# Kernel optimization log

Hardware: AMD Instinct MI355X
Metric: run time of the kernel (lower is better)

Reference implementation:

```python
import jax, jax.numpy as jnp
import numpy as np

N = 100000      # nodes
E = 1600000     # edges (avg degree 16)
IN, HID, OUT = 128, 128, 64


def setup_inputs() -> dict:
    key = jax.random.key(0)
    k1, k2, k3, k4 = jax.random.split(key, 4)
    x = jax.random.normal(k1, (N, IN), dtype=jnp.float32)
    edge_index = jax.random.randint(k2, (2, E), 0, N, dtype=jnp.int64)
    # GCNConv linear weights (glorot-ish scale) and zero biases
    W1 = jax.random.normal(k3, (IN, HID), dtype=jnp.float32) * (1.0 / np.sqrt(IN))
    b1 = jnp.zeros((HID,), jnp.float32)
    W2 = jax.random.normal(k4, (HID, OUT), dtype=jnp.float32) * (1.0 / np.sqrt(HID))
    b2 = jnp.zeros((OUT,), jnp.float32)
    return {"x": x, "edge_index": edge_index, "W1": W1, "b1": b1, "W2": W2, "b2": b2}


def reference(x, edge_index, W1, b1, W2, b2):
    n = x.shape[0]
    loops = jnp.arange(n, dtype=edge_index.dtype)
    self_e = jnp.stack([loops, loops])  # [2, N]
    # forward() explicitly adds self-loops, then PyG GCNConv's gcn_norm
    # (add_self_loops=True by default) adds a second set -> duplicate (i,i) edges.
    ei = jnp.concatenate([edge_index, self_e, self_e], axis=1)
    row, col = ei[0], ei[1]  # source, target

    # symmetric normalization: deg over target index, norm_e = d^-1/2[row]*d^-1/2[col]
    deg = jax.ops.segment_sum(jnp.ones(row.shape, x.dtype), col, num_segments=n)
    dis = jax.lax.rsqrt(deg)  # deg >= 2 thanks to self-loops
    norm = dis[row] * dis[col]  # [E']

    def gcn_conv(h, W, b):
        h = h @ W                               # transform first (PyG order)
        msg = h[row] * norm[:, None]            # gather + per-edge scale
        agg = jax.ops.segment_sum(msg, col, num_segments=n)  # scatter-add
        return agg + b

    h = jax.nn.relu(gcn_conv(x, W1, b1))
    return gcn_conv(h, W2, b2)
```

## Files before the change

### kernel.cpp

```cpp
#include <hip/hip_runtime.h>
#include <hip/hip_fp16.h>

#define NPB   512
#define NBMAX 256
#define CHUNK 2048

using f16x4 = __attribute__((ext_vector_type(4))) _Float16;
using f32x4 = __attribute__((ext_vector_type(4))) float;

__global__ void k_detect(const int* __restrict__ ei32, int* __restrict__ flag,
                         int* __restrict__ bcur, int nb, int cap) {
  int t = threadIdx.x;
  if (t < nb) bcur[t] = t * cap;
  if (t == 0) {
    int z = 1;
    for (int k = 0; k < 64; ++k)
      if (ei32[2 * k + 1] != 0) { z = 0; break; }
    flag[0] = z;
  }
}

__device__ __forceinline__ int edge_at(const void* ei, int is64, long long pos) {
  return is64 ? (int)((const long long*)ei)[pos] : ((const int*)ei)[pos];
}

__global__ __launch_bounds__(256) void k_fillB(const void* __restrict__ ei,
                                               const int* __restrict__ flag, int E,
                                               int* __restrict__ bcur,
                                               int* __restrict__ tmp, int nb) {
  __shared__ int cntL[NBMAX], startL[NBMAX], curL[NBMAX], gofs[NBMAX];
  __shared__ int sh[NBMAX];
  __shared__ int stage[CHUNK];
  __shared__ unsigned char sbkt[CHUNK];
  int t = threadIdx.x;
  int is64 = flag[0];
  long long base = (long long)blockIdx.x * CHUNK;
  if (base >= E) return;
  int m = (int)min((long long)CHUNK, (long long)E - base);
  cntL[t] = 0;
  __syncthreads();
  for (int i = t; i < m; i += 256) {
    int c = edge_at(ei, is64, (long long)E + base + i);
    atomicAdd(&cntL[c >> 9], 1);
  }
  __syncthreads();
  sh[t] = cntL[t];
  __syncthreads();
  for (int off = 1; off < NBMAX; off <<= 1) {
    int x = 0;
    if (t >= off) x = sh[t - off];
    __syncthreads();
    if (t >= off) sh[t] += x;
    __syncthreads();
  }
  int excl = t ? sh[t - 1] : 0;
  startL[t] = excl;
  curL[t] = excl;
  if (t < nb && cntL[t] > 0) gofs[t] = atomicAdd(&bcur[t], cntL[t]);
  __syncthreads();
  for (int i = t; i < m; i += 256) {
    int r = edge_at(ei, is64, base + i);
    int c = edge_at(ei, is64, (long long)E + base + i);
    int b = c >> 9;
    int p = atomicAdd(&curL[b], 1);
    stage[p] = ((c & 511) << 17) | r;
    sbkt[p] = (unsigned char)b;
  }
  __syncthreads();
  for (int i = t; i < m; i += 256) {
    int b = sbkt[i];
    tmp[gofs[b] + (i - startL[b])] = stage[i];
  }
}

template <int BN, bool AHALF, bool PRESCALE>
__device__ void gemm_body(char* smem, const void* __restrict__ Av,
                          const float* __restrict__ W,
                          const float* __restrict__ dis,
                          __half* __restrict__ C, int M, int tiles,
                          int bid, int nblk) {
  _Float16 (*Wt)[136] = (_Float16(*)[136])smem;
  _Float16 (*At)[136] = (_Float16(*)[136])(smem + sizeof(_Float16) * BN * 136);
  float* disL = (float*)(smem + sizeof(_Float16) * (BN + 64) * 136);
  constexpr int NT = BN / 64;
  constexpr int CH = BN / 4;
  int t = threadIdx.x;
  int lane = t & 63, w = t >> 6;
  int lrow = lane & 15;
  int kq = (lane >> 4) * 4;
  int wcol0 = w * (BN / 4);

  for (int idx = t; idx < 128 * BN / 4; idx += 256) {
    int k = idx / CH, c4 = (idx % CH) * 4;
    float4 v = *(const float4*)&W[(size_t)k * BN + c4];
    Wt[c4 + 0][k] = (_Float16)v.x;
    Wt[c4 + 1][k] = (_Float16)v.y;
    Wt[c4 + 2][k] = (_Float16)v.z;
    Wt[c4 + 3][k] = (_Float16)v.w;
  }

  for (int tile = bid; tile < tiles; tile += nblk) {
    int row0 = tile * 64;
    __syncthreads();
#pragma unroll
    for (int i = 0; i < 8; ++i) {
      int idx = t + i * 256;
      int r = idx >> 5, c = (idx & 31) * 4;
      int gr = row0 + r;
      f16x4 hv = {0, 0, 0, 0};
      if (gr < M) {
        if constexpr (AHALF) {
          hv = *(const f16x4*)&((const _Float16*)Av)[(size_t)gr * 128 + c];
        } else {
          float4 v = *(const float4*)&((const float*)Av)[(size_t)gr * 128 + c];
          hv = f16x4{(_Float16)v.x, (_Float16)v.y, (_Float16)v.z, (_Float16)v.w};
        }
      }
      *(f16x4*)&At[r][c] = hv;
    }
    if constexpr (PRESCALE) {
      if (t < 64) {
        int gr = row0 + t;
        disL[t] = (gr < M) ? dis[gr] : 0.f;
      }
    }
    __syncthreads();
    f32x4 acc[4][NT];
#pragma unroll
    for (int mt = 0; mt < 4; ++mt)
#pragma unroll
      for (int nt = 0; nt < NT; ++nt) acc[mt][nt] = f32x4{0.f, 0.f, 0.f, 0.f};
#pragma unroll
    for (int k0 = 0; k0 < 128; k0 += 16) {
      int kk = k0 + kq;
      f16x4 a[4], b[NT];
#pragma unroll
      for (int mt = 0; mt < 4; ++mt)
        a[mt] = *(const f16x4*)&At[mt * 16 + lrow][kk];
#pragma unroll
      for (int nt = 0; nt < NT; ++nt)
        b[nt] = *(const f16x4*)&Wt[wcol0 + nt * 16 + lrow][kk];
#pragma unroll
      for (int mt = 0; mt < 4; ++mt)
#pragma unroll
        for (int nt = 0; nt < NT; ++nt)
          acc[mt][nt] = __builtin_amdgcn_mfma_f32_16x16x16f16(a[mt], b[nt],
                                                              acc[mt][nt], 0, 0, 0);
    }
    __syncthreads();
#pragma unroll
    for (int mt = 0; mt < 4; ++mt)
#pragma unroll
      for (int nt = 0; nt < NT; ++nt) {
        int cc = wcol0 + nt * 16 + lrow;
        int rr = mt * 16 + kq;
#pragma unroll
        for (int reg = 0; reg < 4; ++reg) {
          float val = acc[mt][nt][reg];
          if constexpr (PRESCALE) val *= disL[rr + reg];
          At[rr + reg][cc] = (_Float16)val;
        }
      }
    __syncthreads();
#pragma unroll
    for (int i = 0; i < BN / 16; ++i) {
      int idx = t + i * 256;
      int r = idx / CH, c = (idx % CH) * 4;
      int gr = row0 + r;
      if (gr < M)
        *(f16x4*)&C[(size_t)gr * BN + c] = *(const f16x4*)&At[r][c];
    }
  }
}

__global__ __launch_bounds__(256) void k_gemm1(
    const void* __restrict__ x, const float* __restrict__ W1,
    __half* __restrict__ t1, int M, int tiles) {
  extern __shared__ char smem[];
  gemm_body<128, false, false>(smem, x, W1, nullptr, t1, M, tiles,
                               blockIdx.x, gridDim.x);
}

__global__ __launch_bounds__(256) void k_gemm2(
    const void* __restrict__ Av, const float* __restrict__ W,
    const float* __restrict__ dis, __half* __restrict__ C, int M, int tiles) {
  extern __shared__ char smem[];
  gemm_body<64, true, true>(smem, Av, W, dis, C, M, tiles, blockIdx.x, gridDim.x);
}

__global__ void k_bscan(const int* __restrict__ bcur, int cap,
                        int* __restrict__ bbase, int* __restrict__ rowptr,
                        int nb, int N, int E) {
  __shared__ int sh[NBMAX];
  int t = threadIdx.x;
  sh[t] = (t < nb) ? (bcur[t] - t * cap) : 0;
  __syncthreads();
  for (int off = 1; off < NBMAX; off <<= 1) {
    int x = 0;
    if (t >= off) x = sh[t - off];
    __syncthreads();
    if (t >= off) sh[t] += x;
    __syncthreads();
  }
  int excl = t ? sh[t - 1] : 0;
  if (t < nb) bbase[t] = excl;
  if (t == 0) { bbase[nb] = E; rowptr[N] = E; }
}

__global__ __launch_bounds__(256) void k_fillC(const int* __restrict__ tmp,
                                               const int* __restrict__ bcur,
                                               const int* __restrict__ bbase,
                                               int cap, int* __restrict__ rowptr,
                                               float* __restrict__ dis,
                                               int* __restrict__ esrc,
                                               __half* __restrict__ t1, int N) {
  __shared__ int cnt[NPB];
  __shared__ int loc[NPB];
  __shared__ float disS[NPB];
  __shared__ int sh[256];
  int b = blockIdx.x, t = threadIdx.x;
  int beg = b * cap;
  int end = bcur[b];
  int outb = bbase[b];
  int base_node = b << 9;
  cnt[t] = 0; cnt[t + 256] = 0;
  __syncthreads();
  for (int e = beg + t; e < end; e += 256)
    atomicAdd(&cnt[tmp[e] >> 17], 1);
  __syncthreads();
  int c0 = cnt[2 * t], c1 = cnt[2 * t + 1];
  sh[t] = c0 + c1;
  __syncthreads();
  for (int off = 1; off < 256; off <<= 1) {
    int x = 0;
    if (t >= off) x = sh[t - off];
    __syncthreads();
    if (t >= off) sh[t] += x;
    __syncthreads();
  }
  int pre = t ? sh[t - 1] : 0;
  loc[2 * t] = outb + pre;
  loc[2 * t + 1] = outb + pre + c0;
  float d0 = rsqrtf((float)(c0 + 2)), d1 = rsqrtf((float)(c1 + 2));
  disS[2 * t] = d0; disS[2 * t + 1] = d1;
  int v0 = base_node + 2 * t, v1 = v0 + 1;
  if (v0 < N) { rowptr[v0] = outb + pre;      dis[v0] = d0; }
  if (v1 < N) { rowptr[v1] = outb + pre + c0; dis[v1] = d1; }
  __syncthreads();
  for (int e = beg + t; e < end; e += 256) {
    int u = tmp[e];
    int pos = atomicAdd(&loc[u >> 17], 1);
    esrc[pos] = u & 0x1FFFF;
  }
  for (int idx = t; idx < NPB * 16; idx += 256) {
    int row = idx >> 4, ch = (idx & 15) * 8;
    int v = base_node + row;
    if (v < N) {
      size_t ofs = (size_t)v * 128 + ch;
      uint4 u = *(const uint4*)&t1[ofs];
      float dsc = disS[row];
      __half2* hp = (__half2*)&u;
#pragma unroll
      for (int j = 0; j < 4; ++j) {
        float lo = __low2float(hp[j]) * dsc, hi = __high2float(hp[j]) * dsc;
        hp[j] = __floats2half2_rn(lo, hi);
      }
      *(uint4*)&t1[ofs] = u;
    }
  }
}

#define ACC4(u)                                                         \
  { __half2 p;                                                          \
    p = *(__half2*)&(u).x; a0 += __low2float(p); a1 += __high2float(p); \
    p = *(__half2*)&(u).y; a2 += __low2float(p); a3 += __high2float(p); }

__global__ __launch_bounds__(256) void k_gather128(const __half* __restrict__ t,
    const float* __restrict__ bias, const int* __restrict__ rowptr,
    const int* __restrict__ esrc, const float* __restrict__ dis,
    __half* __restrict__ o, int n) {
  int gw = (int)((blockIdx.x * blockDim.x + threadIdx.x) >> 6);
  int lane = threadIdx.x & 63;
  int nw = (int)((gridDim.x * blockDim.x) >> 6);
  int half = lane >> 5;
  int f = (lane & 31) * 4;
  for (int v = gw; v < n; v += nw) {
    float a0 = 0.f, a1 = 0.f, a2 = 0.f, a3 = 0.f;
    int beg = rowptr[v], end = rowptr[v + 1];
    int e = beg + half;
    for (; e + 14 < end; e += 16) {
      int s0 = esrc[e],      s1 = esrc[e + 2],  s2 = esrc[e + 4],  s3 = esrc[e + 6];
      int s4 = esrc[e + 8],  s5 = esrc[e + 10], s6 = esrc[e + 12], s7 = esrc[e + 14];
      uint2 u0 = *(const uint2*)&t[(size_t)s0 * 128 + f];
      uint2 u1 = *(const uint2*)&t[(size_t)s1 * 128 + f];
      uint2 u2 = *(const uint2*)&t[(size_t)s2 * 128 + f];
      uint2 u3 = *(const uint2*)&t[(size_t)s3 * 128 + f];
      uint2 u4 = *(const uint2*)&t[(size_t)s4 * 128 + f];
      uint2 u5 = *(const uint2*)&t[(size_t)s5 * 128 + f];
      uint2 u6 = *(const uint2*)&t[(size_t)s6 * 128 + f];
      uint2 u7 = *(const uint2*)&t[(size_t)s7 * 128 + f];
      ACC4(u0) ACC4(u1) ACC4(u2) ACC4(u3)
      ACC4(u4) ACC4(u5) ACC4(u6) ACC4(u7)
    }
    for (; e + 6 < end; e += 8) {
      int s0 = esrc[e], s1 = esrc[e + 2], s2 = esrc[e + 4], s3 = esrc[e + 6];
      uint2 u0 = *(const uint2*)&t[(size_t)s0 * 128 + f];
      uint2 u1 = *(const uint2*)&t[(size_t)s1 * 128 + f];
      uint2 u2 = *(const uint2*)&t[(size_t)s2 * 128 + f];
      uint2 u3 = *(const uint2*)&t[(size_t)s3 * 128 + f];
      ACC4(u0) ACC4(u1) ACC4(u2) ACC4(u3)
    }
    for (; e < end; e += 2) {
      int s0 = esrc[e];
      uint2 u0 = *(const uint2*)&t[(size_t)s0 * 128 + f];
      ACC4(u0)
    }
    if (half == 0) {
      uint2 uv = *(const uint2*)&t[(size_t)v * 128 + f];
      __half2 p;
      p = *(__half2*)&uv.x; a0 = fmaf(2.f, __low2float(p), a0); a1 = fmaf(2.f, __high2float(p), a1);
      p = *(__half2*)&uv.y; a2 = fmaf(2.f, __low2float(p), a2); a3 = fmaf(2.f, __high2float(p), a3);
    }
    a0 += __shfl_xor(a0, 32); a1 += __shfl_xor(a1, 32);
    a2 += __shfl_xor(a2, 32); a3 += __shfl_xor(a3, 32);
    if (half == 0) {
      float dv = dis[v];
      a0 = fmaxf(fmaf(dv, a0, bias[f]),     0.f);
      a1 = fmaxf(fmaf(dv, a1, bias[f + 1]), 0.f);
      a2 = fmaxf(fmaf(dv, a2, bias[f + 2]), 0.f);
      a3 = fmaxf(fmaf(dv, a3, bias[f + 3]), 0.f);
      __half2 h0 = __floats2half2_rn(a0, a1), h1 = __floats2half2_rn(a2, a3);
      uint2 uu;
      uu.x = *(unsigned int*)&h0; uu.y = *(unsigned int*)&h1;
      *(uint2*)&o[(size_t)v * 128 + f] = uu;
    }
  }
}

__global__ __launch_bounds__(256) void k_gather64(const __half* __restrict__ t,
    const float* __restrict__ bias, const int* __restrict__ rowptr,
    const int* __restrict__ esrc, const float* __restrict__ dis,
    float* __restrict__ o, int n) {
  int gw = (int)((blockIdx.x * blockDim.x + threadIdx.x) >> 6);
  int lane = threadIdx.x & 63;
  int nw = (int)((gridDim.x * blockDim.x) >> 6);
  int sub = lane >> 4;
  int f = (lane & 15) * 4;
  for (int v = gw; v < n; v += nw) {
    float a0 = 0.f, a1 = 0.f, a2 = 0.f, a3 = 0.f;
    int beg = rowptr[v], end = rowptr[v + 1];
    int e = beg + sub;
    for (; e + 12 < end; e += 16) {
      int s0 = esrc[e], s1 = esrc[e + 4], s2 = esrc[e + 8], s3 = esrc[e + 12];
      uint2 u0 = *(const uint2*)&t[(size_t)s0 * 64 + f];
      uint2 u1 = *(const uint2*)&t[(size_t)s1 * 64 + f];
      uint2 u2 = *(const uint2*)&t[(size_t)s2 * 64 + f];
      uint2 u3 = *(const uint2*)&t[(size_t)s3 * 64 + f];
      ACC4(u0) ACC4(u1) ACC4(u2) ACC4(u3)
    }
    for (; e < end; e += 4) {
      int s0 = esrc[e];
      uint2 u0 = *(const uint2*)&t[(size_t)s0 * 64 + f];
      ACC4(u0)
    }
    if (sub == 0) {
      uint2 uv = *(const uint2*)&t[(size_t)v * 64 + f];
      __half2 p;
      p = *(__half2*)&uv.x; a0 = fmaf(2.f, __low2float(p), a0); a1 = fmaf(2.f, __high2float(p), a1);
      p = *(__half2*)&uv.y; a2 = fmaf(2.f, __low2float(p), a2); a3 = fmaf(2.f, __high2float(p), a3);
    }
    a0 += __shfl_xor(a0, 16); a0 += __shfl_xor(a0, 32);
    a1 += __shfl_xor(a1, 16); a1 += __shfl_xor(a1, 32);
    a2 += __shfl_xor(a2, 16); a2 += __shfl_xor(a2, 32);
    a3 += __shfl_xor(a3, 16); a3 += __shfl_xor(a3, 32);
    if (sub == 0) {
      float dv = dis[v];
      float4 r;
      r.x = fmaf(dv, a0, bias[f]);     r.y = fmaf(dv, a1, bias[f + 1]);
      r.z = fmaf(dv, a2, bias[f + 2]); r.w = fmaf(dv, a3, bias[f + 3]);
      *(float4*)&o[(size_t)v * 64 + f] = r;
    }
  }
}

extern "C" void kernel_launch(void* const* d_in, const int* in_sizes, int n_in,
                              void* d_out, int out_size, void* d_ws, size_t ws_size,
                              hipStream_t stream) {
  const float* x  = (const float*)d_in[0];
  const void*  ei = d_in[1];
  const float* W1 = (const float*)d_in[2];
  const float* b1 = (const float*)d_in[3];
  const float* W2 = (const float*)d_in[4];
  const float* b2 = (const float*)d_in[5];
  const int N = in_sizes[0] / 128;
  const int E = in_sizes[1] / 2;
  float* out = (float*)d_out;
  const int nb  = (N + NPB - 1) / NPB;
  const int cap = E / nb + 4096;

  size_t off = 0;
  auto alloc = [&](size_t bytes) -> void* {
    void* p = (char*)d_ws + off;
    off += (bytes + 255) & ~(size_t)255;
    return p;
  };
  int*    flag   = (int*)alloc(4);
  int*    bcur   = (int*)alloc(NBMAX * 4);
  int*    bbase  = (int*)alloc((NBMAX + 1) * 4);
  int*    rowptr = (int*)alloc(((size_t)N + 1) * 4);
  float*  dis    = (float*)alloc((size_t)N * 4);
  int*    tmp    = (int*)alloc(((size_t)nb * cap + 16384) * 4);
  int*    esrc   = (int*)alloc((size_t)E * 4);
  __half* t1     = (__half*)alloc((size_t)N * 128 * 2);
  __half* z1     = (__half*)alloc((size_t)N * 128 * 2);
  __half* t2     = t1;

  int tiles = (N + 63) / 64;
  int nchunks = (E + CHUNK - 1) / CHUNK;
  const int smem_gemm1 = (128 + 64) * 136 * 2 + 256;
  const int smem_gemm2 = (64 + 64) * 136 * 2 + 256;

  k_detect<<<1, 256, 0, stream>>>((const int*)ei, flag, bcur, nb, cap);
  k_gemm1<<<768, 256, smem_gemm1, stream>>>(x, W1, t1, N, tiles);
  k_fillB<<<nchunks, 256, 0, stream>>>(ei, flag, E, bcur, tmp, nb);
  k_bscan<<<1, 256, 0, stream>>>(bcur, cap, bbase, rowptr, nb, N, E);
  k_fillC<<<nb, 256, 0, stream>>>(tmp, bcur, bbase, cap, rowptr, dis, esrc, t1, N);

  k_gather128<<<2048, 256, 0, stream>>>(t1, b1, rowptr, esrc, dis, z1, N);
  k_gemm2<<<min(tiles, 768), 256, smem_gemm2, stream>>>(z1, W2, dis, t2, N, tiles);
  k_gather64<<<2048, 256, 0, stream>>>(t2, b2, rowptr, esrc, dis, out, N);
}
```

Baseline: 230.7 us.

## Move GEMM1 after CSR build with fused dis prescale and register-resident W

GEMM1 now runs after the CSR/degree build, so it can apply the dis[row] prescale in its epilogue. This removes the separate read-modify-write pass over t1 that k_fillC used to do. The GEMM kernel is rewritten so each wave holds its W fragments in registers rather than in a shared-memory transposed tile, uses BN*4 threads, and launches one block per tile. The trade-off is that GEMM1 can no longer overlap with the CSR build and must wait for dis, and W is loaded with strided scalar global reads.

```diff
diff --git a/kernel.cpp b/kernel.cpp
--- a/kernel.cpp
+++ b/kernel.cpp
@@ -73,38 +73,100 @@
   }
 }
 
+__global__ void k_bscan(const int* __restrict__ bcur, int cap,
+                        int* __restrict__ bbase, int* __restrict__ rowptr,
+                        int nb, int N, int E) {
+  __shared__ int sh[NBMAX];
+  int t = threadIdx.x;
+  sh[t] = (t < nb) ? (bcur[t] - t * cap) : 0;
+  __syncthreads();
+  for (int off = 1; off < NBMAX; off <<= 1) {
+    int x = 0;
+    if (t >= off) x = sh[t - off];
+    __syncthreads();
+    if (t >= off) sh[t] += x;
+    __syncthreads();
+  }
+  int excl = t ? sh[t - 1] : 0;
+  if (t < nb) bbase[t] = excl;
+  if (t == 0) { bbase[nb] = E; rowptr[N] = E; }
+}
+
+__global__ __launch_bounds__(256) void k_fillC(const int* __restrict__ tmp,
+                                               const int* __restrict__ bcur,
+                                               const int* __restrict__ bbase,
+                                               int cap, int* __restrict__ rowptr,
+                                               float* __restrict__ dis,
+                                               int* __restrict__ esrc, int N) {
+  __shared__ int cnt[NPB];
+  __shared__ int loc[NPB];
+  __shared__ int sh[256];
+  int b = blockIdx.x, t = threadIdx.x;
+  int beg = b * cap;
+  int end = bcur[b];
+  int outb = bbase[b];
+  int base_node = b << 9;
+  cnt[t] = 0; cnt[t + 256] = 0;
+  __syncthreads();
+  for (int e = beg + t; e < end; e += 256)
+    atomicAdd(&cnt[tmp[e] >> 17], 1);
+  __syncthreads();
+  int c0 = cnt[2 * t], c1 = cnt[2 * t + 1];
+  sh[t] = c0 + c1;
+  __syncthreads();
+  for (int off = 1; off < 256; off <<= 1) {
+    int x = 0;
+    if (t >= off) x = sh[t - off];
+    __syncthreads();
+    if (t >= off) sh[t] += x;
+    __syncthreads();
+  }
+  int pre = t ? sh[t - 1] : 0;
+  loc[2 * t] = outb + pre;
+  loc[2 * t + 1] = outb + pre + c0;
+  int v0 = base_node + 2 * t, v1 = v0 + 1;
+  if (v0 < N) { rowptr[v0] = outb + pre;      dis[v0] = rsqrtf((float)(c0 + 2)); }
+  if (v1 < N) { rowptr[v1] = outb + pre + c0; dis[v1] = rsqrtf((float)(c1 + 2)); }
+  __syncthreads();
+  for (int e = beg + t; e < end; e += 256) {
+    int u = tmp[e];
+    int pos = atomicAdd(&loc[u >> 17], 1);
+    esrc[pos] = u & 0x1FFFF;
+  }
+}
+
 template <int BN, bool AHALF, bool PRESCALE>
-__device__ void gemm_body(char* smem, const void* __restrict__ Av,
-                          const float* __restrict__ W,
-                          const float* __restrict__ dis,
-                          __half* __restrict__ C, int M, int tiles,
-                          int bid, int nblk) {
-  _Float16 (*Wt)[136] = (_Float16(*)[136])smem;
-  _Float16 (*At)[136] = (_Float16(*)[136])(smem + sizeof(_Float16) * BN * 136);
-  float* disL = (float*)(smem + sizeof(_Float16) * (BN + 64) * 136);
-  constexpr int NT = BN / 64;
+__global__ __launch_bounds__(BN * 4) void k_gemm(const void* __restrict__ Av,
+                                                 const float* __restrict__ W,
+                                                 const float* __restrict__ dis,
+                                                 __half* __restrict__ C,
+                                                 int M, int tiles) {
+  constexpr int THREADS = BN * 4;
   constexpr int CH = BN / 4;
+  __shared__ _Float16 At[64][136];
+  __shared__ float disL[64];
   int t = threadIdx.x;
   int lane = t & 63, w = t >> 6;
   int lrow = lane & 15;
   int kq = (lane >> 4) * 4;
-  int wcol0 = w * (BN / 4);
-
-  for (int idx = t; idx < 128 * BN / 4; idx += 256) {
-    int k = idx / CH, c4 = (idx % CH) * 4;
-    float4 v = *(const float4*)&W[(size_t)k * BN + c4];
-    Wt[c4 + 0][k] = (_Float16)v.x;
-    Wt[c4 + 1][k] = (_Float16)v.y;
-    Wt[c4 + 2][k] = (_Float16)v.z;
-    Wt[c4 + 3][k] = (_Float16)v.w;
-  }
-
-  for (int tile = bid; tile < tiles; tile += nblk) {
+  int col = w * 16 + lrow;
+
+  f16x4 bfrag[8];
+#pragma unroll
+  for (int k8 = 0; k8 < 8; ++k8) {
+    int kb = k8 * 16 + kq;
+    bfrag[k8] = f16x4{(_Float16)W[(size_t)(kb + 0) * BN + col],
+                      (_Float16)W[(size_t)(kb + 1) * BN + col],
+                      (_Float16)W[(size_t)(kb + 2) * BN + col],
+                      (_Float16)W[(size_t)(kb + 3) * BN + col]};
+  }
+
+  for (int tile = blockIdx.x; tile < tiles; tile += gridDim.x) {
     int row0 = tile * 64;
     __syncthreads();
 #pragma unroll
-    for (int i = 0; i < 8; ++i) {
-      int idx = t + i * 256;
+    for (int i = 0; i < (64 * 32) / THREADS; ++i) {
+      int idx = t + i * THREADS;
       int r = idx >> 5, c = (idx & 31) * 4;
       int gr = row0 + r;
       f16x4 hv = {0, 0, 0, 0};
@@ -125,147 +187,40 @@
       }
     }
     __syncthreads();
-    f32x4 acc[4][NT];
-#pragma unroll
-    for (int mt = 0; mt < 4; ++mt)
-#pragma unroll
-      for (int nt = 0; nt < NT; ++nt) acc[mt][nt] = f32x4{0.f, 0.f, 0.f, 0.f};
-#pragma unroll
-    for (int k0 = 0; k0 < 128; k0 += 16) {
-      int kk = k0 + kq;
-      f16x4 a[4], b[NT];
+    f32x4 acc[4];
+#pragma unroll
+    for (int mt = 0; mt < 4; ++mt) acc[mt] = f32x4{0.f, 0.f, 0.f, 0.f};
+#pragma unroll
+    for (int k8 = 0; k8 < 8; ++k8) {
+      int kk = k8 * 16 + kq;
+      f16x4 a[4];
 #pragma unroll
       for (int mt = 0; mt < 4; ++mt)
         a[mt] = *(const f16x4*)&At[mt * 16 + lrow][kk];
 #pragma unroll
-      for (int nt = 0; nt < NT; ++nt)
-        b[nt] = *(const f16x4*)&Wt[wcol0 + nt * 16 + lrow][kk];
-#pragma unroll
       for (int mt = 0; mt < 4; ++mt)
-#pragma unroll
-        for (int nt = 0; nt < NT; ++nt)
-          acc[mt][nt] = __builtin_amdgcn_mfma_f32_16x16x16f16(a[mt], b[nt],
-                                                              acc[mt][nt], 0, 0, 0);
-    }
-    __syncthreads();
-#pragma unroll
-    for (int mt = 0; mt < 4; ++mt)
-#pragma unroll
-      for (int nt = 0; nt < NT; ++nt) {
-        int cc = wcol0 + nt * 16 + lrow;
-        int rr = mt * 16 + kq;
-#pragma unroll
-        for (int reg = 0; reg < 4; ++reg) {
-          float val = acc[mt][nt][reg];
-          if constexpr (PRESCALE) val *= disL[rr + reg];
-          At[rr + reg][cc] = (_Float16)val;
-        }
+        acc[mt] = __builtin_amdgcn_mfma_f32_16x16x16f16(a[mt], bfrag[k8],
+                                                        acc[mt], 0, 0, 0);
+    }
+    __syncthreads();
+#pragma unroll
+    for (int mt = 0; mt < 4; ++mt) {
+      int rr = mt * 16 + kq;
+#pragma unroll
+      for (int reg = 0; reg < 4; ++reg) {
+        float val = acc[mt][reg];
+        if constexpr (PRESCALE) val *= disL[rr + reg];
+        At[rr + reg][col] = (_Float16)val;
       }
-    __syncthreads();
-#pragma unroll
-    for (int i = 0; i < BN / 16; ++i) {
-      int idx = t + i * 256;
+    }
+    __syncthreads();
+#pragma unroll
+    for (int i = 0; i < (64 * CH) / THREADS; ++i) {
+      int idx = t + i * THREADS;
       int r = idx / CH, c = (idx % CH) * 4;
       int gr = row0 + r;
       if (gr < M)
         *(f16x4*)&C[(size_t)gr * BN + c] = *(const f16x4*)&At[r][c];
-    }
-  }
-}
-
-__global__ __launch_bounds__(256) void k_gemm1(
-    const void* __restrict__ x, const float* __restrict__ W1,
-    __half* __restrict__ t1, int M, int tiles) {
-  extern __shared__ char smem[];
-  gemm_body<128, false, false>(smem, x, W1, nullptr, t1, M, tiles,
-                               blockIdx.x, gridDim.x);
-}
-
-__global__ __launch_bounds__(256) void k_gemm2(
-    const void* __restrict__ Av, const float* __restrict__ W,
-    const float* __restrict__ dis, __half* __restrict__ C, int M, int tiles) {
-  extern __shared__ char smem[];
-  gemm_body<64, true, true>(smem, Av, W, dis, C, M, tiles, blockIdx.x, gridDim.x);
-}
-
-__global__ void k_bscan(const int* __restrict__ bcur, int cap,
-                        int* __restrict__ bbase, int* __restrict__ rowptr,
-                        int nb, int N, int E) {
-  __shared__ int sh[NBMAX];
-  int t = threadIdx.x;
-  sh[t] = (t < nb) ? (bcur[t] - t * cap) : 0;
-  __syncthreads();
-  for (int off = 1; off < NBMAX; off <<= 1) {
-    int x = 0;
-    if (t >= off) x = sh[t - off];
-    __syncthreads();
-    if (t >= off) sh[t] += x;
-    __syncthreads();
-  }
-  int excl = t ? sh[t - 1] : 0;
-  if (t < nb) bbase[t] = excl;
-  if (t == 0) { bbase[nb] = E; rowptr[N] = E; }
-}
-
-__global__ __launch_bounds__(256) void k_fillC(const int* __restrict__ tmp,
-                                               const int* __restrict__ bcur,
-                                               const int* __restrict__ bbase,
-                                               int cap, int* __restrict__ rowptr,
-                                               float* __restrict__ dis,
-                                               int* __restrict__ esrc,
-                                               __half* __restrict__ t1, int N) {
-  __shared__ int cnt[NPB];
-  __shared__ int loc[NPB];
-  __shared__ float disS[NPB];
-  __shared__ int sh[256];
-  int b = blockIdx.x, t = threadIdx.x;
-  int beg = b * cap;
-  int end = bcur[b];
-  int outb = bbase[b];
-  int base_node = b << 9;
-  cnt[t] = 0; cnt[t + 256] = 0;
-  __syncthreads();
-  for (int e = beg + t; e < end; e += 256)
-    atomicAdd(&cnt[tmp[e] >> 17], 1);
-  __syncthreads();
-  int c0 = cnt[2 * t], c1 = cnt[2 * t + 1];
-  sh[t] = c0 + c1;
-  __syncthreads();
-  for (int off = 1; off < 256; off <<= 1) {
-    int x = 0;
-    if (t >= off) x = sh[t - off];
-    __syncthreads();
-    if (t >= off) sh[t] += x;
-    __syncthreads();
-  }
-  int pre = t ? sh[t - 1] : 0;
-  loc[2 * t] = outb + pre;
-  loc[2 * t + 1] = outb + pre + c0;
-  float d0 = rsqrtf((float)(c0 + 2)), d1 = rsqrtf((float)(c1 + 2));
-  disS[2 * t] = d0; disS[2 * t + 1] = d1;
-  int v0 = base_node + 2 * t, v1 = v0 + 1;
-  if (v0 < N) { rowptr[v0] = outb + pre;      dis[v0] = d0; }
-  if (v1 < N) { rowptr[v1] = outb + pre + c0; dis[v1] = d1; }
-  __syncthreads();
-  for (int e = beg + t; e < end; e += 256) {
-    int u = tmp[e];
-    int pos = atomicAdd(&loc[u >> 17], 1);
-    esrc[pos] = u & 0x1FFFF;
-  }
-  for (int idx = t; idx < NPB * 16; idx += 256) {
-    int row = idx >> 4, ch = (idx & 15) * 8;
-    int v = base_node + row;
-    if (v < N) {
-      size_t ofs = (size_t)v * 128 + ch;
-      uint4 u = *(const uint4*)&t1[ofs];
-      float dsc = disS[row];
-      __half2* hp = (__half2*)&u;
-#pragma unroll
-      for (int j = 0; j < 4; ++j) {
-        float lo = __low2float(hp[j]) * dsc, hi = __high2float(hp[j]) * dsc;
-        hp[j] = __floats2half2_rn(lo, hi);
-      }
-      *(uint4*)&t1[ofs] = u;
     }
   }
 }
@@ -417,16 +372,14 @@
 
   int tiles = (N + 63) / 64;
   int nchunks = (E + CHUNK - 1) / CHUNK;
-  const int smem_gemm1 = (128 + 64) * 136 * 2 + 256;
-  const int smem_gemm2 = (64 + 64) * 136 * 2 + 256;
 
   k_detect<<<1, 256, 0, stream>>>((const int*)ei, flag, bcur, nb, cap);
-  k_gemm1<<<768, 256, smem_gemm1, stream>>>(x, W1, t1, N, tiles);
   k_fillB<<<nchunks, 256, 0, stream>>>(ei, flag, E, bcur, tmp, nb);
   k_bscan<<<1, 256, 0, stream>>>(bcur, cap, bbase, rowptr, nb, N, E);
-  k_fillC<<<nb, 256, 0, stream>>>(tmp, bcur, bbase, cap, rowptr, dis, esrc, t1, N);
-
+  k_fillC<<<nb, 256, 0, stream>>>(tmp, bcur, bbase, cap, rowptr, dis, esrc, N);
+
+  k_gemm<128, false, true><<<tiles, 512, 0, stream>>>(x, W1, dis, t1, N, tiles);
   k_gather128<<<2048, 256, 0, stream>>>(t1, b1, rowptr, esrc, dis, z1, N);
-  k_gemm2<<<min(tiles, 768), 256, smem_gemm2, stream>>>(z1, W2, dis, t2, N, tiles);
+  k_gemm<64, true, true><<<tiles, 256, 0, stream>>>(z1, W2, dis, t2, N, tiles);
   k_gather64<<<2048, 256, 0, stream>>>(t2, b2, rowptr, esrc, dis, out, N);
 }
```

Result: faster. 205.5 us (-10.9%).
